# Optimization experiments

Measured on AMD Instinct MI355X. Metric: run time of the kernel, lower is better.

The kernel has to match this reference:

```python
import jax, jax.numpy as jnp
import numpy as np

N = 8192   # nodes
D = 128    # uniform feature dim (arch = [128,128,128])
L = 2      # num_layers = len(arch)-1
EDGE_P = 0.01

def setup_inputs() -> dict:
    key = jax.random.key(0)
    ks = jax.random.split(key, 11)
    features = jax.random.normal(ks[0], (N, D), dtype=jnp.float32)
    # sparse symmetric adjacency with self-loops (diagonal forced True, as in forward)
    a = jax.random.uniform(ks[1], (N, N)) < EDGE_P
    mask = a | a.T | jnp.eye(N, dtype=bool)
    s = 1.0 / np.sqrt(D)
    def w(k):
        return (jax.random.normal(k, (L, D, D), dtype=jnp.float32) * s)
    def b(k):
        return jax.random.normal(k, (L, D), dtype=jnp.float32) * 0.01
    return {
        "features": features, "mask": mask,
        "Wq": w(ks[2]), "bq": b(ks[3]),
        "Wk": w(ks[4]), "bk": b(ks[5]),
        "Wv": w(ks[6]), "bv": b(ks[7]),
        "Wo": w(ks[8]), "bo": b(ks[9]),
    }

def reference(features, mask, Wq, bq, Wk, bk, Wv, bv, Wo, bo):
    h = features
    outputs = [h]
    for l in range(L):
        Q = h @ Wq[l] + bq[l]                      # [N, D]
        K = h @ Wk[l] + bk[l]
        V = h @ Wv[l] + bv[l]
        scores = (Q @ K.T) * (1.0 / jnp.sqrt(jnp.float32(K.shape[1])))  # [N, N]
        scores = jnp.where(mask, scores, -jnp.inf)
        attn = jax.nn.softmax(scores, axis=1)
        h = attn @ V                                # [N, D]
        h = h @ Wo[l] + bo[l]
        outputs.append(h)
    return tuple(outputs)
```

## Files before the change

kernel.cpp:

```cpp
#include <hip/hip_runtime.h>
#include <hip/hip_bf16.h>
#include <hip/hip_fp16.h>
#include <math.h>

#define N 8192
#define D 128
#define CAP 512

typedef _Float16 f16x2 __attribute__((ext_vector_type(2)));
typedef _Float16 f16x4 __attribute__((ext_vector_type(4)));
typedef _Float16 f16x8 __attribute__((ext_vector_type(8)));

__device__ __forceinline__ float dot2(f16x2 a, f16x2 b, float c) {
#if __has_builtin(__builtin_amdgcn_fdot2)
    return __builtin_amdgcn_fdot2(a, b, c, false);
#else
    return c + (float)a[0] * (float)b[0] + (float)a[1] * (float)b[1];
#endif
}

__device__ __forceinline__ float dot8(f16x8 a, f16x8 b, float c) {
    c = dot2(__builtin_shufflevector(a, a, 0, 1), __builtin_shufflevector(b, b, 0, 1), c);
    c = dot2(__builtin_shufflevector(a, a, 2, 3), __builtin_shufflevector(b, b, 2, 3), c);
    c = dot2(__builtin_shufflevector(a, a, 4, 5), __builtin_shufflevector(b, b, 4, 5), c);
    c = dot2(__builtin_shufflevector(a, a, 6, 7), __builtin_shufflevector(b, b, 6, 7), c);
    return c;
}

__global__ __launch_bounds__(256) void build_adj(const int* __restrict__ mask,
                                                 unsigned short* __restrict__ nbr,
                                                 int* __restrict__ deg) {
    const int i = blockIdx.x;
    __shared__ int cnt;
    if (threadIdx.x == 0) cnt = 0;
    __syncthreads();
    const int4* row = (const int4*)(mask + (size_t)i * N);
    for (int c = threadIdx.x; c < N / 4; c += 256) {
        int4 m4 = row[c];
        int base = 4 * c;
        if (m4.x) { int p = atomicAdd(&cnt, 1); if (p < CAP) nbr[(size_t)i * CAP + p] = (unsigned short)(base); }
        if (m4.y) { int p = atomicAdd(&cnt, 1); if (p < CAP) nbr[(size_t)i * CAP + p] = (unsigned short)(base + 1); }
        if (m4.z) { int p = atomicAdd(&cnt, 1); if (p < CAP) nbr[(size_t)i * CAP + p] = (unsigned short)(base + 2); }
        if (m4.w) { int p = atomicAdd(&cnt, 1); if (p < CAP) nbr[(size_t)i * CAP + p] = (unsigned short)(base + 3); }
    }
    __syncthreads();
    if (threadIdx.x == 0) deg[i] = (cnt > CAP) ? CAP : cnt;
}

__global__ __launch_bounds__(256) void qkv_gemm(const float* __restrict__ A,
                                                const float* __restrict__ Wq, const float* __restrict__ bq,
                                                const float* __restrict__ Wk, const float* __restrict__ bk,
                                                const float* __restrict__ Wv, const float* __restrict__ bv,
                                                __half* __restrict__ Qo, __half* __restrict__ Ko,
                                                __half* __restrict__ Vo,
                                                float* __restrict__ copy_out) {
    __shared__ float As[8][D];
    const int tid = threadIdx.x;
    const int r   = tid >> 5;
    const int jg  = tid & 31;
    const int i0  = blockIdx.x * 8;

    const float4 av = ((const float4*)(A + (size_t)i0 * D))[tid];
    ((float4*)&As[0][0])[tid] = av;
    ((float4*)(copy_out + (size_t)i0 * D))[tid] = av;
    __syncthreads();

    const float* Ws[3] = {Wq, Wk, Wv};
    const float* bs[3] = {bq, bk, bv};
    __half* Os[3] = {Qo, Ko, Vo};
    const size_t st[3] = {D, 2 * D, 2 * D};

    #pragma unroll
    for (int m = 0; m < 3; ++m) {
        float4 acc = *(const float4*)(bs[m] + 4 * jg);
        const float* W = Ws[m];
        #pragma unroll 8
        for (int k4 = 0; k4 < 32; ++k4) {
            const float4 a4 = *(const float4*)&As[r][4 * k4];
            const float* wb = W + (size_t)(4 * k4) * D + 4 * jg;
            const float4 w0 = *(const float4*)(wb);
            const float4 w1 = *(const float4*)(wb + D);
            const float4 w2 = *(const float4*)(wb + 2 * D);
            const float4 w3 = *(const float4*)(wb + 3 * D);
            acc.x += a4.x * w0.x + a4.y * w1.x + a4.z * w2.x + a4.w * w3.x;
            acc.y += a4.x * w0.y + a4.y * w1.y + a4.z * w2.y + a4.w * w3.y;
            acc.z += a4.x * w0.z + a4.y * w1.z + a4.z * w2.z + a4.w * w3.z;
            acc.w += a4.x * w0.w + a4.y * w1.w + a4.z * w2.w + a4.w * w3.w;
        }
        f16x4 h;
        h[0] = (_Float16)acc.x; h[1] = (_Float16)acc.y;
        h[2] = (_Float16)acc.z; h[3] = (_Float16)acc.w;
        *(f16x4*)(Os[m] + (size_t)(i0 + r) * st[m] + 4 * jg) = h;
    }
}

__global__ __launch_bounds__(256) void gemmO_qkv(const float* __restrict__ Aattn,
                                                 const float* __restrict__ Wo, const float* __restrict__ bo,
                                                 float* __restrict__ Hout,
                                                 const float* __restrict__ Wq, const float* __restrict__ bq,
                                                 const float* __restrict__ Wk, const float* __restrict__ bk,
                                                 const float* __restrict__ Wv, const float* __restrict__ bv,
                                                 __half* __restrict__ Qo, __half* __restrict__ Ko,
                                                 __half* __restrict__ Vo) {
    __shared__ float As[8][D];
    __shared__ float Hs[8][D];
    const int tid = threadIdx.x;
    const int r   = tid >> 5;
    const int jg  = tid & 31;
    const int i0  = blockIdx.x * 8;

    ((float4*)&As[0][0])[tid] = ((const float4*)(Aattn + (size_t)i0 * D))[tid];
    __syncthreads();

    {
        float4 acc = *(const float4*)(bo + 4 * jg);
        #pragma unroll 8
        for (int k4 = 0; k4 < 32; ++k4) {
            const float4 a4 = *(const float4*)&As[r][4 * k4];
            const float* wb = Wo + (size_t)(4 * k4) * D + 4 * jg;
            const float4 w0 = *(const float4*)(wb);
            const float4 w1 = *(const float4*)(wb + D);
            const float4 w2 = *(const float4*)(wb + 2 * D);
            const float4 w3 = *(const float4*)(wb + 3 * D);
            acc.x += a4.x * w0.x + a4.y * w1.x + a4.z * w2.x + a4.w * w3.x;
            acc.y += a4.x * w0.y + a4.y * w1.y + a4.z * w2.y + a4.w * w3.y;
            acc.z += a4.x * w0.z + a4.y * w1.z + a4.z * w2.z + a4.w * w3.z;
            acc.w += a4.x * w0.w + a4.y * w1.w + a4.z * w2.w + a4.w * w3.w;
        }
        *(float4*)(Hout + (size_t)(i0 + r) * D + 4 * jg) = acc;
        *(float4*)&Hs[r][4 * jg] = acc;
    }
    __syncthreads();

    const float* Ws[3] = {Wq, Wk, Wv};
    const float* bs[3] = {bq, bk, bv};
    __half* Os[3] = {Qo, Ko, Vo};
    const size_t st[3] = {D, 2 * D, 2 * D};
    #pragma unroll
    for (int m = 0; m < 3; ++m) {
        float4 acc = *(const float4*)(bs[m] + 4 * jg);
        const float* W = Ws[m];
        #pragma unroll 8
        for (int k4 = 0; k4 < 32; ++k4) {
            const float4 a4 = *(const float4*)&Hs[r][4 * k4];
            const float* wb = W + (size_t)(4 * k4) * D + 4 * jg;
            const float4 w0 = *(const float4*)(wb);
            const float4 w1 = *(const float4*)(wb + D);
            const float4 w2 = *(const float4*)(wb + 2 * D);
            const float4 w3 = *(const float4*)(wb + 3 * D);
            acc.x += a4.x * w0.x + a4.y * w1.x + a4.z * w2.x + a4.w * w3.x;
            acc.y += a4.x * w0.y + a4.y * w1.y + a4.z * w2.y + a4.w * w3.y;
            acc.z += a4.x * w0.z + a4.y * w1.z + a4.z * w2.z + a4.w * w3.z;
            acc.w += a4.x * w0.w + a4.y * w1.w + a4.z * w2.w + a4.w * w3.w;
        }
        f16x4 h;
        h[0] = (_Float16)acc.x; h[1] = (_Float16)acc.y;
        h[2] = (_Float16)acc.z; h[3] = (_Float16)acc.w;
        *(f16x4*)(Os[m] + (size_t)(i0 + r) * st[m] + 4 * jg) = h;
    }
}

__global__ __launch_bounds__(256) void gemm_bias(const float* __restrict__ A,
                                                 const float* __restrict__ W,
                                                 const float* __restrict__ bias,
                                                 float* __restrict__ C) {
    __shared__ float As[8][D];
    const int tid = threadIdx.x;
    const int r   = tid >> 5;
    const int jg  = tid & 31;
    const int i0  = blockIdx.x * 8;

    ((float4*)&As[0][0])[tid] = ((const float4*)(A + (size_t)i0 * D))[tid];
    __syncthreads();

    float4 acc = *(const float4*)(bias + 4 * jg);
    #pragma unroll 8
    for (int k4 = 0; k4 < 32; ++k4) {
        const float4 a4 = *(const float4*)&As[r][4 * k4];
        const float* wb = W + (size_t)(4 * k4) * D + 4 * jg;
        const float4 w0 = *(const float4*)(wb);
        const float4 w1 = *(const float4*)(wb + D);
        const float4 w2 = *(const float4*)(wb + 2 * D);
        const float4 w3 = *(const float4*)(wb + 3 * D);
        acc.x += a4.x * w0.x + a4.y * w1.x + a4.z * w2.x + a4.w * w3.x;
        acc.y += a4.x * w0.y + a4.y * w1.y + a4.z * w2.y + a4.w * w3.y;
        acc.z += a4.x * w0.z + a4.y * w1.z + a4.z * w2.z + a4.w * w3.z;
        acc.w += a4.x * w0.w + a4.y * w1.w + a4.z * w2.w + a4.w * w3.w;
    }
    *(float4*)(C + (size_t)(i0 + r) * D + 4 * jg) = acc;
}

__global__ __launch_bounds__(256) void attn_sparse(const __half* __restrict__ Q,
                                                   const __half* __restrict__ KV,
                                                   const unsigned short* __restrict__ nbr,
                                                   const int* __restrict__ deg,
                                                   float* __restrict__ Hout) {
    const int tid  = threadIdx.x;
    const int wave = tid >> 6;
    const int lane = tid & 63;
    const int g    = lane >> 4;
    const int gl   = lane & 15;
    const int i    = blockIdx.x * 4 + wave;

    __shared__ unsigned short jls[4][CAP];

    const int dg = min(deg[i], CAP);
    for (int e = lane; e < dg; e += 64)
        jls[wave][e] = nbr[(size_t)i * CAP + e];
    const f16x8 qv = ((const f16x8*)(Q + (size_t)i * D))[gl];
    __syncthreads();

    const float scale = 0.088388347648318447f;

    float acc[8] = {0.f, 0.f, 0.f, 0.f, 0.f, 0.f, 0.f, 0.f};
    float denom  = 0.f;

    #pragma unroll 1
    for (int ph = 0; ph < 4; ++ph) {
        for (int e = g; e < dg; e += 4) {
            const int j = jls[wave][e];
            if ((j >> 11) != ph) continue;
            const f16x8* kvp = (const f16x8*)(KV + (size_t)j * (2 * D));
            const f16x8 kv = kvp[gl];
            const f16x8 v8 = kvp[16 + gl];
            float dot = dot8(kv, qv, 0.f);
            dot += __shfl_xor(dot, 1);
            dot += __shfl_xor(dot, 2);
            dot += __shfl_xor(dot, 4);
            dot += __shfl_xor(dot, 8);
            const float p = __expf(dot * scale);
            #pragma unroll
            for (int k = 0; k < 8; ++k) acc[k] += p * (float)v8[k];
            denom += p;
        }
    }

    #pragma unroll
    for (int k = 0; k < 8; ++k) {
        acc[k] += __shfl_xor(acc[k], 16);
        acc[k] += __shfl_xor(acc[k], 32);
    }
    denom += __shfl_xor(denom, 16);
    denom += __shfl_xor(denom, 32);

    if (g == 0) {
        const float inv = 1.0f / denom;
        float4 o0, o1;
        o0.x = acc[0] * inv; o0.y = acc[1] * inv; o0.z = acc[2] * inv; o0.w = acc[3] * inv;
        o1.x = acc[4] * inv; o1.y = acc[5] * inv; o1.z = acc[6] * inv; o1.w = acc[7] * inv;
        float4* dst = (float4*)(Hout + (size_t)i * D + 8 * gl);
        dst[0] = o0;
        dst[1] = o1;
    }
}

extern "C" void kernel_launch(void* const* d_in, const int* in_sizes, int n_in,
                              void* d_out, int out_size, void* d_ws, size_t ws_size,
                              hipStream_t stream) {
    const float* features = (const float*)d_in[0];
    const int*   mask     = (const int*)d_in[1];
    const float* Wq = (const float*)d_in[2];
    const float* bq = (const float*)d_in[3];
    const float* Wk = (const float*)d_in[4];
    const float* bk = (const float*)d_in[5];
    const float* Wv = (const float*)d_in[6];
    const float* bv = (const float*)d_in[7];
    const float* Wo = (const float*)d_in[8];
    const float* bo = (const float*)d_in[9];
    float* out = (float*)d_out;

    char* base = (char*)d_ws;
    unsigned short* nbr = (unsigned short*)base;
    int*    deg  = (int*)(base + (size_t)N * CAP * 2);
    __half* Qb16 = (__half*)(base + (size_t)N * CAP * 2 + N * 4);
    __half* KVb  = Qb16 + (size_t)N * D;
    float*  tmp  = (float*)(KVb + (size_t)N * 2 * D);

    build_adj<<<N, 256, 0, stream>>>(mask, nbr, deg);

    qkv_gemm<<<N / 8, 256, 0, stream>>>(features, Wq, bq, Wk, bk, Wv, bv,
                                        Qb16, KVb, KVb + D, out);
    attn_sparse<<<N / 4, 256, 0, stream>>>(Qb16, KVb, nbr, deg, tmp);
    gemmO_qkv<<<N / 8, 256, 0, stream>>>(tmp, Wo, bo, out + (size_t)N * D,
                                         Wq + D * D, bq + D, Wk + D * D, bk + D,
                                         Wv + D * D, bv + D, Qb16, KVb, KVb + D);
    attn_sparse<<<N / 4, 256, 0, stream>>>(Qb16, KVb, nbr, deg, tmp);
    gemm_bias<<<N / 8, 256, 0, stream>>>(tmp, Wo + D * D, bo + D,
                                         out + (size_t)2 * N * D);
}
```

Measured before the change: 615.8 us.

## Software-pipeline neighbor K/V loads and drop phase-ordered traversal in sparse attention

After: 574.7 us. -6.7%, faster.

```diff
diff --git a/kernel.cpp b/kernel.cpp
--- a/kernel.cpp
+++ b/kernel.cpp
@@ -10,6 +10,7 @@
 typedef _Float16 f16x2 __attribute__((ext_vector_type(2)));
 typedef _Float16 f16x4 __attribute__((ext_vector_type(4)));
 typedef _Float16 f16x8 __attribute__((ext_vector_type(8)));
+typedef float    f32x4 __attribute__((ext_vector_type(4)));
 
 __device__ __forceinline__ float dot2(f16x2 a, f16x2 b, float c) {
 #if __has_builtin(__builtin_amdgcn_fdot2)
@@ -19,12 +20,12 @@
 #endif
 }
 
-__device__ __forceinline__ float dot8(f16x8 a, f16x8 b, float c) {
-    c = dot2(__builtin_shufflevector(a, a, 0, 1), __builtin_shufflevector(b, b, 0, 1), c);
-    c = dot2(__builtin_shufflevector(a, a, 2, 3), __builtin_shufflevector(b, b, 2, 3), c);
-    c = dot2(__builtin_shufflevector(a, a, 4, 5), __builtin_shufflevector(b, b, 4, 5), c);
-    c = dot2(__builtin_shufflevector(a, a, 6, 7), __builtin_shufflevector(b, b, 6, 7), c);
-    return c;
+__device__ __forceinline__ float dot8(f16x8 a, f16x8 b) {
+    float c0 = dot2(__builtin_shufflevector(a, a, 0, 1), __builtin_shufflevector(b, b, 0, 1), 0.f);
+    float c1 = dot2(__builtin_shufflevector(a, a, 2, 3), __builtin_shufflevector(b, b, 2, 3), 0.f);
+    c0 = dot2(__builtin_shufflevector(a, a, 4, 5), __builtin_shufflevector(b, b, 4, 5), c0);
+    c1 = dot2(__builtin_shufflevector(a, a, 6, 7), __builtin_shufflevector(b, b, 6, 7), c1);
+    return c0 + c1;
 }
 
 __global__ __launch_bounds__(256) void build_adj(const int* __restrict__ mask,
@@ -206,7 +207,7 @@
 
     const int dg = min(deg[i], CAP);
     for (int e = lane; e < dg; e += 64)
-        jls[wave][e] = nbr[(size_t)i * CAP + e];
+        jls[wave][e] = __builtin_nontemporal_load(&nbr[(size_t)i * CAP + e]);
     const f16x8 qv = ((const f16x8*)(Q + (size_t)i * D))[gl];
     __syncthreads();
 
@@ -215,24 +216,30 @@
     float acc[8] = {0.f, 0.f, 0.f, 0.f, 0.f, 0.f, 0.f, 0.f};
     float denom  = 0.f;
 
-    #pragma unroll 1
-    for (int ph = 0; ph < 4; ++ph) {
-        for (int e = g; e < dg; e += 4) {
-            const int j = jls[wave][e];
-            if ((j >> 11) != ph) continue;
-            const f16x8* kvp = (const f16x8*)(KV + (size_t)j * (2 * D));
-            const f16x8 kv = kvp[gl];
-            const f16x8 v8 = kvp[16 + gl];
-            float dot = dot8(kv, qv, 0.f);
-            dot += __shfl_xor(dot, 1);
-            dot += __shfl_xor(dot, 2);
-            dot += __shfl_xor(dot, 4);
-            dot += __shfl_xor(dot, 8);
-            const float p = __expf(dot * scale);
-            #pragma unroll
-            for (int k = 0; k < 8; ++k) acc[k] += p * (float)v8[k];
-            denom += p;
-        }
+    int e = g;
+    int jc = (e < dg) ? (int)jls[wave][e] : 0;
+    const f16x8* kvp = (const f16x8*)(KV + (size_t)jc * (2 * D));
+    f16x8 kc = kvp[gl];
+    f16x8 vc = kvp[16 + gl];
+
+    while (e < dg) {
+        const int en = e + 4;
+        const int jn = (en < dg) ? (int)jls[wave][en] : 0;
+        const f16x8* kvpn = (const f16x8*)(KV + (size_t)jn * (2 * D));
+        const f16x8 kn = kvpn[gl];
+        const f16x8 vn = kvpn[16 + gl];
+
+        float dot = dot8(kc, qv);
+        dot += __shfl_xor(dot, 1);
+        dot += __shfl_xor(dot, 2);
+        dot += __shfl_xor(dot, 4);
+        dot += __shfl_xor(dot, 8);
+        const float p = __expf(dot * scale);
+        #pragma unroll
+        for (int k = 0; k < 8; ++k) acc[k] += p * (float)vc[k];
+        denom += p;
+
+        e = en; kc = kn; vc = vn;
     }
 
     #pragma unroll
@@ -245,12 +252,12 @@
 
     if (g == 0) {
         const float inv = 1.0f / denom;
-        float4 o0, o1;
-        o0.x = acc[0] * inv; o0.y = acc[1] * inv; o0.z = acc[2] * inv; o0.w = acc[3] * inv;
-        o1.x = acc[4] * inv; o1.y = acc[5] * inv; o1.z = acc[6] * inv; o1.w = acc[7] * inv;
-        float4* dst = (float4*)(Hout + (size_t)i * D + 8 * gl);
-        dst[0] = o0;
-        dst[1] = o1;
+        f32x4 o0, o1;
+        o0[0] = acc[0] * inv; o0[1] = acc[1] * inv; o0[2] = acc[2] * inv; o0[3] = acc[3] * inv;
+        o1[0] = acc[4] * inv; o1[1] = acc[5] * inv; o1[2] = acc[6] * inv; o1[3] = acc[7] * inv;
+        f32x4* dst = (f32x4*)(Hout + (size_t)i * D + 8 * gl);
+        __builtin_nontemporal_store(o0, &dst[0]);
+        __builtin_nontemporal_store(o1, &dst[1]);
     }
 }
 
```
